# Kernel tuning notes

Hardware: AMD Instinct MI355X
Metric: run time of the kernel (lower is better)

## Reference

```python
import jax, jax.numpy as jnp
import numpy as np

B, L, D, H = 2, 1024, 512, 8
h = D // H            # head_dim = 64
K = H                 # num_eigh must equal num_heads (vmap pairing in conv)
EPS = 1e-5


def _spectral_filters(seq_len: int, k: int) -> np.ndarray:
    # Hankel matrix Z_{ij} = 2 / ((i+j)^3 - (i+j)), top-k eigenvectors scaled by sigma^{1/4}
    e = np.arange(1, seq_len + 1, dtype=np.float64)
    ipj = e[:, None] + e[None, :]
    Z = 2.0 / (ipj ** 3 - ipj)
    sigma, phi = np.linalg.eigh(Z)
    sigma_k = np.clip(sigma[-k:], 1e-9, None)
    return (phi[:, -k:] * sigma_k ** 0.25).astype(np.float32)  # [L, K]


def setup_inputs() -> dict:
    key = jax.random.key(0)
    ks = jax.random.split(key, 8)
    s = 0.02
    return {
        "x": jax.random.normal(ks[0], (B, L, D), jnp.float32),
        "spectral_basis": jnp.asarray(_spectral_filters(L, K)),       # [L, K]
        "wq_w": jax.random.normal(ks[1], (D, D), jnp.float32) * s,
        "wq_b": jnp.zeros((D,), jnp.float32),
        "wk_w": jax.random.normal(ks[2], (D, D), jnp.float32) * s,
        "wk_b": jnp.zeros((D,), jnp.float32),
        "wv_w": jax.random.normal(ks[3], (D, D), jnp.float32) * s,
        "wv_b": jnp.zeros((D,), jnp.float32),
        "wo_w": jax.random.normal(ks[4], (D, D), jnp.float32) * s,
        "wo_b": jnp.zeros((D,), jnp.float32),
        "wg_w": jax.random.normal(ks[5], (h * h,), jnp.float32) * s,  # Linear(h^2 -> 1)
        "wg_b": jnp.zeros((), jnp.float32),
    }


def _causal_fft_conv(u, filt_f, n):
    # u: [B,H,L,h]; filt_f: precomputed rfft of per-head filters [H, F]
    Uf = jnp.fft.rfft(u, n=n, axis=2)                        # [B,H,F,h]
    y = jnp.fft.irfft(Uf * filt_f[None, :, :, None], n=n, axis=2)
    return y[:, :, :L]                                       # truncate full conv -> causal


def reference(x, spectral_basis, wq_w, wq_b, wk_w, wk_b, wv_w, wv_b,
              wo_w, wo_b, wg_w, wg_b):
    # projections -> [B,H,L,h]
    q = (x @ wq_w + wq_b).reshape(B, L, H, h).transpose(0, 2, 1, 3)
    k = (x @ wk_w + wk_b).reshape(B, L, H, h).transpose(0, 2, 1, 3) * h ** (-0.5)
    v = (x @ wv_w + wv_b).reshape(B, L, H, h).transpose(0, 2, 1, 3)

    n = 2 * L
    filt_f = jnp.fft.rfft(spectral_basis.T, n=n, axis=1)     # [H, F] (one filter per head)
    k_conv = _causal_fft_conv(k, filt_f, n)
    v_conv = _causal_fft_conv(v, filt_f, n)

    # gated outer product Z: [B,H,L,h,h]
    Z = jnp.einsum('bhlm,bhln->bhlmn', v_conv, k_conv)
    gate_logits = Z.reshape(B, H, L, h * h) @ wg_w + wg_b    # [B,H,L]
    gates = jax.nn.relu(gate_logits) ** 2 + EPS
    gated_Z = gates[..., None, None] * Z

    # associative scan (additive) over sequence dim
    cumul_gated_Z = jnp.cumsum(gated_Z, axis=2)              # [B,H,L,h,h]
    cumul_gates = jnp.cumsum(gates, axis=2)                  # [B,H,L]
    attn = cumul_gated_Z / (cumul_gates[..., None, None] + EPS)

    # note: original einsum sums over l (and d) independently of s
    ctxt = jnp.einsum('bhsd,bhlde->bhse', q, attn)           # [B,H,L,h]
    norm = jnp.linalg.norm(ctxt, axis=3, keepdims=True)
    unit = ctxt / jnp.maximum(norm, EPS)                     # F.normalize semantics
    out = unit.transpose(0, 2, 1, 3).reshape(B, L, D)
    return out @ wo_w + wo_b
```

## Files before the change

kernel.cpp:

```cpp
#include <hip/hip_runtime.h>
#include <math.h>


typedef __attribute__((ext_vector_type(8))) short short8;
typedef __attribute__((ext_vector_type(4))) float floatx4;

__device__ __forceinline__ unsigned short f2bf(float f) {
    unsigned int u = __float_as_uint(f);
    unsigned int r = (u + 0x7FFFu + ((u >> 16) & 1u)) >> 16;
    return (unsigned short)r;
}

__global__ __launch_bounds__(256) void k_prep(
    const float* __restrict__ x,
    const float* __restrict__ wq, const float* __restrict__ wk,
    const float* __restrict__ wv, const float* __restrict__ wo,
    const float* __restrict__ wg,
    unsigned short* __restrict__ xb,
    unsigned short* __restrict__ wT, unsigned short* __restrict__ woT,
    unsigned short* __restrict__ wgb)
{
    __shared__ float sf[64][65];
    const int blk = blockIdx.x;
    const int tid = threadIdx.x;

    if (blk < 512) {
        const int gid = blk * 256 + tid;
        const float4* x4 = (const float4*)x;
        float4 a = x4[gid*2], b = x4[gid*2+1];
        uint4 o;
        o.x = f2bf(a.x) | ((unsigned)f2bf(a.y) << 16);
        o.y = f2bf(a.z) | ((unsigned)f2bf(a.w) << 16);
        o.z = f2bf(b.x) | ((unsigned)f2bf(b.y) << 16);
        o.w = f2bf(b.z) | ((unsigned)f2bf(b.w) << 16);
        ((uint4*)xb)[gid] = o;
    } else if (blk < 768) {
        const int t = blk - 512;
        const float* src; unsigned short* dst; int n0, c0, k0;
        if (t < 192) {
            int nt = t >> 3, kt = t & 7;
            n0 = nt * 64; k0 = kt * 64;
            int z = n0 >> 9; c0 = n0 & 511;
            src = (z == 0) ? wq : (z == 1) ? wk : wv;
            dst = wT;
        } else {
            int u = t - 192; int nt = u >> 3, kt = u & 7;
            n0 = nt * 64; c0 = n0; k0 = kt * 64;
            src = wo; dst = woT;
        }
        const int rr = tid >> 4, c4 = tid & 15;
        #pragma unroll
        for (int g = 0; g < 4; ++g) {
            int r = g*16 + rr;
            float4 v = *(const float4*)&src[(size_t)(k0 + r)*512 + c0 + c4*4];
            sf[r][c4*4+0]=v.x; sf[r][c4*4+1]=v.y; sf[r][c4*4+2]=v.z; sf[r][c4*4+3]=v.w;
        }
        __syncthreads();
        #pragma unroll
        for (int g = 0; g < 4; ++g) {
            int c = g*16 + rr;
            int kk = c4*4;
            ushort4 o;
            o.x = f2bf(sf[kk+0][c]); o.y = f2bf(sf[kk+1][c]);
            o.z = f2bf(sf[kk+2][c]); o.w = f2bf(sf[kk+3][c]);
            *(ushort4*)&dst[(size_t)(n0 + c)*512 + k0 + kk] = o;
        }
    } else {
        const float4* wg4 = (const float4*)wg;
        for (int i = tid; i < 512; i += 256) {
            float4 a = wg4[i*2], b = wg4[i*2+1];
            uint4 o;
            o.x = f2bf(a.x) | ((unsigned)f2bf(a.y) << 16);
            o.y = f2bf(a.z) | ((unsigned)f2bf(a.w) << 16);
            o.z = f2bf(b.x) | ((unsigned)f2bf(b.y) << 16);
            o.w = f2bf(b.z) | ((unsigned)f2bf(b.w) << 16);
            ((uint4*)wgb)[i] = o;
        }
    }
}

__global__ __launch_bounds__(256) void k_qkv_mfma(
    const unsigned short* __restrict__ xb, const unsigned short* __restrict__ wT,
    const float* __restrict__ bq, const float* __restrict__ bk,
    const float* __restrict__ bv,
    float* __restrict__ qo, unsigned short* __restrict__ ub2)
{
    const int tid = threadIdx.x;
    const int lane = tid & 63, wave = tid >> 6;
    const int q = lane >> 4, ln = lane & 15;
    const int wm = wave * 32;
    const int m0 = blockIdx.y * 128;
    const int n0 = blockIdx.x * 64;

    __shared__ unsigned short As[128*72];
    __shared__ unsigned short Bs[64*72];

    floatx4 acc[2][4];
    #pragma unroll
    for (int i = 0; i < 2; ++i)
        #pragma unroll
        for (int j = 0; j < 4; ++j)
            acc[i][j] = (floatx4){0.f, 0.f, 0.f, 0.f};

    const uint4* Ag = (const uint4*)xb;
    const uint4* Bg = (const uint4*)wT;
    for (int k0 = 0; k0 < 512; k0 += 64) {
        #pragma unroll
        for (int s = 0; s < 4; ++s) {
            int idx = s*256 + tid;
            int r = idx >> 3, cp = idx & 7;
            uint4 va = Ag[(size_t)(m0 + r)*64 + (k0 >> 3) + cp];
            *(uint4*)&As[r*72 + cp*8] = va;
        }
        #pragma unroll
        for (int s = 0; s < 2; ++s) {
            int idx = s*256 + tid;
            int r = idx >> 3, cp = idx & 7;
            uint4 vb = Bg[(size_t)(n0 + r)*64 + (k0 >> 3) + cp];
            *(uint4*)&Bs[r*72 + cp*8] = vb;
        }
        __syncthreads();
        short8 af0[2], af1[2], bf0[4], bf1[4];
        #pragma unroll
        for (int i = 0; i < 2; ++i) {
            af0[i] = *(const short8*)&As[(wm + i*16 + ln)*72 + q*8];
            af1[i] = *(const short8*)&As[(wm + i*16 + ln)*72 + 32 + q*8];
        }
        #pragma unroll
        for (int i = 0; i < 4; ++i) {
            bf0[i] = *(const short8*)&Bs[(i*16 + ln)*72 + q*8];
            bf1[i] = *(const short8*)&Bs[(i*16 + ln)*72 + 32 + q*8];
        }
        #pragma unroll
        for (int mi = 0; mi < 2; ++mi)
            #pragma unroll
            for (int ni = 0; ni < 4; ++ni) {
                acc[mi][ni] = __builtin_amdgcn_mfma_f32_16x16x32_bf16(
                    af0[mi], bf0[ni], acc[mi][ni], 0, 0, 0);
                acc[mi][ni] = __builtin_amdgcn_mfma_f32_16x16x32_bf16(
                    af1[mi], bf1[ni], acc[mi][ni], 0, 0, 0);
            }
        __syncthreads();
    }

    const int z = n0 >> 9;
    if (z == 0) {
        #pragma unroll
        for (int mi = 0; mi < 2; ++mi) {
            #pragma unroll
            for (int ni = 0; ni < 4; ++ni) {
                int c = (n0 + ni*16 + ln) & 511;
                int head = c >> 6, dd = c & 63;
                float bb = bq[c];
                #pragma unroll
                for (int reg = 0; reg < 4; ++reg) {
                    int row = m0 + wm + mi*16 + q*4 + reg;
                    int b = row >> 10, l = row & 1023;
                    qo[(size_t)((b*8 + head)*1024 + l)*64 + dd] =
                        acc[mi][ni][reg] + bb;
                }
            }
        }
    } else {
        const float scale = (z == 1) ? 0.125f : 1.0f;
        const float* bias = (z == 1) ? bk : bv;
        unsigned short* dst = ub2 + (size_t)(z-1) * 16 * 64 * 1024;
        #pragma unroll
        for (int mi = 0; mi < 2; ++mi) {
            #pragma unroll
            for (int ni = 0; ni < 4; ++ni) {
                int c = (n0 + ni*16 + ln) & 511;
                int head = c >> 6, dd = c & 63;
                float bb = bias[c];
                int row0 = m0 + wm + mi*16 + q*4;
                int b = row0 >> 10, l0 = row0 & 1023;
                ushort4 o;
                o.x = f2bf((acc[mi][ni][0] + bb) * scale);
                o.y = f2bf((acc[mi][ni][1] + bb) * scale);
                o.z = f2bf((acc[mi][ni][2] + bb) * scale);
                o.w = f2bf((acc[mi][ni][3] + bb) * scale);
                *(ushort4*)&dst[((size_t)((b*8 + head)*64) + dd)*1024 + l0] = o;
            }
        }
    }
}

__global__ __launch_bounds__(256) void k_conv_mfma(
    const float* __restrict__ sb,
    const unsigned short* __restrict__ ub2,
    float* __restrict__ kc, float* __restrict__ vc,
    unsigned short* __restrict__ kcb)
{
    const int tid = threadIdx.x;
    const int lane = tid & 63, wave = tid >> 6;
    const int q = lane >> 4, ln = lane & 15;
    const int bht = blockIdx.x;
    const int it  = blockIdx.y;
    const int t0  = it * 64;
    const int bh  = bht & 15, h = bh & 7, tensor = bht >> 4;

    __shared__ unsigned short revf[1152];
    __shared__ unsigned short Bs[64*72];

    for (int i = tid; i < 1152; i += 256) {
        int d = 1087 - i;
        revf[i] = (d >= 0 && d < 1024) ? f2bf(sb[d*8 + h]) : (unsigned short)0;
    }

    const uint4* Bg = (const uint4*)ub2;
    const size_t bbase = (size_t)bht * 8192;

    floatx4 acc[4];
    #pragma unroll
    for (int i = 0; i < 4; ++i) acc[i] = (floatx4){0.f,0.f,0.f,0.f};

    const int kend = t0 + 64;
    const int arow = 1087 - t0 - (wave*16 + ln);
    for (int k0 = 0; k0 < kend; k0 += 64) {
        #pragma unroll
        for (int s = 0; s < 2; ++s) {
            int idx = s*256 + tid;
            int r = idx >> 3, cp = idx & 7;
            uint4 vb = Bg[bbase + (size_t)r*128 + (k0 >> 3) + cp];
            *(uint4*)&Bs[r*72 + cp*8] = vb;
        }
        __syncthreads();
        const int ab = arow + k0 + q*8;
        short8 a0, a1;
        #pragma unroll
        for (int j = 0; j < 8; ++j) {
            a0[j] = (short)revf[ab + j];
            a1[j] = (short)revf[ab + 32 + j];
        }
        #pragma unroll
        for (int ni = 0; ni < 4; ++ni) {
            short8 b0 = *(const short8*)&Bs[(ni*16 + ln)*72 + q*8];
            short8 b1 = *(const short8*)&Bs[(ni*16 + ln)*72 + 32 + q*8];
            acc[ni] = __builtin_amdgcn_mfma_f32_16x16x32_bf16(a0, b0, acc[ni], 0, 0, 0);
            acc[ni] = __builtin_amdgcn_mfma_f32_16x16x32_bf16(a1, b1, acc[ni], 0, 0, 0);
        }
        __syncthreads();
    }

    float* dst = (tensor ? vc : kc) + (size_t)bh * 65536;
    #pragma unroll
    for (int ni = 0; ni < 4; ++ni)
        #pragma unroll
        for (int reg = 0; reg < 4; ++reg) {
            int row = t0 + wave*16 + q*4 + reg;
            dst[(size_t)row*64 + ni*16 + ln] = acc[ni][reg];
        }
    if (!tensor) {
        unsigned short* db = kcb + (size_t)bh * 65536;
        #pragma unroll
        for (int ni = 0; ni < 4; ++ni)
            #pragma unroll
            for (int reg = 0; reg < 4; ++reg) {
                int row = t0 + wave*16 + q*4 + reg;
                db[(size_t)row*64 + ni*16 + ln] = f2bf(acc[ni][reg]);
            }
    }
}

__global__ __launch_bounds__(256) void k_gate_mfma(
    const unsigned short* __restrict__ kcb, const float* __restrict__ vc,
    const unsigned short* __restrict__ wgb, const float* __restrict__ wg_b,
    float* __restrict__ gl)
{
    const int tid = threadIdx.x;
    const int lane = tid & 63, wave = tid >> 6;
    const int q = lane >> 4, ln = lane & 15;
    const int l0 = blockIdx.x * 64;
    const int bh = blockIdx.y;

    __shared__ unsigned short As[64*72];
    __shared__ unsigned short Bs[64*72];

    const uint4* Ag = (const uint4*)(kcb + (size_t)bh * 65536);
    const uint4* Bg = (const uint4*)wgb;
    #pragma unroll
    for (int s = 0; s < 2; ++s) {
        int idx = s*256 + tid;
        int r = idx >> 3, cp = idx & 7;
        *(uint4*)&As[r*72 + cp*8] = Ag[(size_t)(l0 + r)*8 + cp];
        *(uint4*)&Bs[r*72 + cp*8] = Bg[r*8 + cp];
    }
    __syncthreads();

    floatx4 T[4];
    #pragma unroll
    for (int mt = 0; mt < 4; ++mt) T[mt] = (floatx4){0.f,0.f,0.f,0.f};
    #pragma unroll
    for (int k0 = 0; k0 < 64; k0 += 32) {
        short8 a = *(const short8*)&As[(wave*16 + ln)*72 + k0 + q*8];
        #pragma unroll
        for (int mt = 0; mt < 4; ++mt) {
            short8 b = *(const short8*)&Bs[(mt*16 + ln)*72 + k0 + q*8];
            T[mt] = __builtin_amdgcn_mfma_f32_16x16x32_bf16(a, b, T[mt], 0, 0, 0);
        }
    }

    const float* vb = vc + (size_t)bh * 65536;
    float part[4] = {0.f, 0.f, 0.f, 0.f};
    #pragma unroll
    for (int mt = 0; mt < 4; ++mt)
        #pragma unroll
        for (int reg = 0; reg < 4; ++reg) {
            int l = l0 + wave*16 + q*4 + reg;
            part[reg] += T[mt][reg] * vb[(size_t)l*64 + mt*16 + ln];
        }
    #pragma unroll
    for (int reg = 0; reg < 4; ++reg) {
        part[reg] += __shfl_xor(part[reg], 1);
        part[reg] += __shfl_xor(part[reg], 2);
        part[reg] += __shfl_xor(part[reg], 4);
        part[reg] += __shfl_xor(part[reg], 8);
    }
    if (ln == 0) {
        const float wgbias = wg_b[0];
        #pragma unroll
        for (int reg = 0; reg < 4; ++reg) {
            int l = l0 + wave*16 + q*4 + reg;
            float s = part[reg] + wgbias;
            float rr = fmaxf(s, 0.0f);
            gl[bh*1024 + l] = rr*rr + 1e-5f;
        }
    }
}

__global__ __launch_bounds__(256) void k_amat(
    const float* __restrict__ kc, const float* __restrict__ vc,
    const float* __restrict__ gl, float* __restrict__ apart)
{
    const int tid = threadIdx.x, tx = tid & 15, ty = tid >> 4;
    const int bh = blockIdx.x, slc = blockIdx.y;
    const float* kb = kc + (size_t)bh * 65536;
    const float* vb = vc + (size_t)bh * 65536;

    __shared__ float sbuf[256];
    __shared__ float wfull[1024];
    __shared__ __align__(16) float vs[16][68];
    __shared__ __align__(16) float ks2[16][68];

    {
        const float4 g4 = ((const float4*)(gl + bh*1024))[tid];
        float g[4] = {g4.x, g4.y, g4.z, g4.w};
        float p[4];
        p[0]=g[0]; p[1]=p[0]+g[1]; p[2]=p[1]+g[2]; p[3]=p[2]+g[3];
        const float s = p[3];
        sbuf[tid] = s;
        __syncthreads();
        for (int off = 1; off < 256; off <<= 1) {
            float t = (tid >= off) ? sbuf[tid-off] : 0.0f;
            __syncthreads();
            sbuf[tid] += t;
            __syncthreads();
        }
        const float base = sbuf[tid] - s;
        float r[4], pr[4];
        #pragma unroll
        for (int u = 0; u < 4; ++u) r[u] = 1.0f / (base + p[u] + 1e-5f);
        pr[0]=r[0]; pr[1]=pr[0]+r[1]; pr[2]=pr[1]+r[2]; pr[3]=pr[2]+r[3];
        const float sr = pr[3];
        __syncthreads();
        sbuf[tid] = sr;
        __syncthreads();
        for (int off = 1; off < 256; off <<= 1) {
            float t = (tid >= off) ? sbuf[tid-off] : 0.0f;
            __syncthreads();
            sbuf[tid] += t;
            __syncthreads();
        }
        const float Rtot  = sbuf[255];
        const float baser = sbuf[tid] - sr;
        wfull[tid*4+0] = g[0] * (Rtot - (baser + pr[0]) + r[0]);
        wfull[tid*4+1] = g[1] * (Rtot - (baser + pr[1]) + r[1]);
        wfull[tid*4+2] = g[2] * (Rtot - (baser + pr[2]) + r[2]);
        wfull[tid*4+3] = g[3] * (Rtot - (baser + pr[3]) + r[3]);
    }
    __syncthreads();

    float acc[4][4] = {};
    const float4* k4 = (const float4*)kb;
    const float4* v4 = (const float4*)vb;
    for (int j0 = slc*128; j0 < slc*128 + 128; j0 += 16) {
        {
            int r = tid >> 4, c4 = tid & 15;
            *(float4*)&vs[r][c4*4]  = v4[(size_t)(j0 + r)*16 + c4];
            *(float4*)&ks2[r][c4*4] = k4[(size_t)(j0 + r)*16 + c4];
        }
        __syncthreads();
        #pragma unroll
        for (int jj = 0; jj < 16; ++jj) {
            float wj = wfull[j0 + jj];
            float a[4];
            a[0] = vs[jj][ty*4+0]*wj; a[1] = vs[jj][ty*4+1]*wj;
            a[2] = vs[jj][ty*4+2]*wj; a[3] = vs[jj][ty*4+3]*wj;
            float4 b4 = *(const float4*)&ks2[jj][tx*4];
            float bb[4] = {b4.x, b4.y, b4.z, b4.w};
            #pragma unroll
            for (int ii = 0; ii < 4; ++ii)
                #pragma unroll
                for (int jc = 0; jc < 4; ++jc)
                    acc[ii][jc] += a[ii] * bb[jc];
        }
        __syncthreads();
    }
    float* ap = apart + (size_t)(slc*16 + bh) * 4096;
    #pragma unroll
    for (int i = 0; i < 4; ++i) {
        float4 o = { acc[i][0], acc[i][1], acc[i][2], acc[i][3] };
        *(float4*)&ap[(ty*4+i)*64 + tx*4] = o;
    }
}

__global__ __launch_bounds__(256) void k_ctxt(
    const float* __restrict__ q, const float* __restrict__ apart,
    unsigned short* __restrict__ ub)
{
    const int tid = threadIdx.x, tx = tid & 15, ty = tid >> 4;
    const int l0 = blockIdx.x * 64;
    const int bh = blockIdx.y;
    const float* qb = q + (size_t)bh * 65536;

    __shared__ __align__(16) float qs[64][20];
    __shared__ __align__(16) float As[16][68];
    float acc[4][4] = {};
    const float4* q4 = (const float4*)qb;
    const float4* a4 = (const float4*)apart;
    for (int d0 = 0; d0 < 64; d0 += 16) {
        {
            int r = tid >> 2, c4 = tid & 3;
            float4 t = q4[(size_t)(l0 + r)*16 + (d0 >> 2) + c4];
            *(float4*)&qs[r][c4*4] = t;
        }
        {
            int r = tid >> 4, c4 = tid & 15;
            size_t o = (size_t)(d0 + r)*16 + c4;
            float4 t = a4[(size_t)(0*16 + bh)*1024 + o];
            #pragma unroll
            for (int s = 1; s < 8; ++s) {
                float4 u = a4[(size_t)(s*16 + bh)*1024 + o];
                t.x += u.x; t.y += u.y; t.z += u.z; t.w += u.w;
            }
            *(float4*)&As[r][c4*4] = t;
        }
        __syncthreads();
        float qreg[4][16];
        #pragma unroll
        for (int i = 0; i < 4; ++i)
            #pragma unroll
            for (int c = 0; c < 4; ++c) {
                float4 t = *(const float4*)&qs[ty*4+i][c*4];
                qreg[i][c*4+0] = t.x; qreg[i][c*4+1] = t.y;
                qreg[i][c*4+2] = t.z; qreg[i][c*4+3] = t.w;
            }
        #pragma unroll
        for (int dd = 0; dd < 16; ++dd) {
            float4 b4 = *(const float4*)&As[dd][tx*4];
            float bb[4] = {b4.x, b4.y, b4.z, b4.w};
            #pragma unroll
            for (int ii = 0; ii < 4; ++ii)
                #pragma unroll
                for (int jj = 0; jj < 4; ++jj)
                    acc[ii][jj] += qreg[ii][dd] * bb[jj];
        }
        __syncthreads();
    }
    __shared__ float red[64][17];
    __shared__ float nrm[64];
    #pragma unroll
    for (int i = 0; i < 4; ++i) {
        red[ty*4+i][tx] = acc[i][0]*acc[i][0] + acc[i][1]*acc[i][1]
                        + acc[i][2]*acc[i][2] + acc[i][3]*acc[i][3];
    }
    __syncthreads();
    if (tid < 64) {
        float s = 0.0f;
        #pragma unroll
        for (int t = 0; t < 16; ++t) s += red[tid][t];
        nrm[tid] = fmaxf(sqrtf(s), 1e-5f);
    }
    __syncthreads();
    const int b = bh >> 3, hd = bh & 7;
    #pragma unroll
    for (int i = 0; i < 4; ++i) {
        int lr = ty*4 + i;
        float inv = 1.0f / nrm[lr];
        ushort4 o;
        o.x = f2bf(acc[i][0]*inv); o.y = f2bf(acc[i][1]*inv);
        o.z = f2bf(acc[i][2]*inv); o.w = f2bf(acc[i][3]*inv);
        *(ushort4*)&ub[(size_t)(b*1024 + l0 + lr)*512 + hd*64 + tx*4] = o;
    }
}

__global__ __launch_bounds__(256) void k_out_mfma(
    const unsigned short* __restrict__ ub, const unsigned short* __restrict__ woT,
    const float* __restrict__ bo, float* __restrict__ out)
{
    const int tid = threadIdx.x;
    const int lane = tid & 63, wave = tid >> 6;
    const int q = lane >> 4, ln = lane & 15;
    const int wm = wave * 32;
    const int m0 = blockIdx.y * 128;
    const int n0 = blockIdx.x * 64;

    __shared__ unsigned short As[128*72];
    __shared__ unsigned short Bs[64*72];

    floatx4 acc[2][4];
    #pragma unroll
    for (int i = 0; i < 2; ++i)
        #pragma unroll
        for (int j = 0; j < 4; ++j)
            acc[i][j] = (floatx4){0.f, 0.f, 0.f, 0.f};

    const uint4* Ag = (const uint4*)ub;
    const uint4* Bg = (const uint4*)woT;
    for (int k0 = 0; k0 < 512; k0 += 64) {
        #pragma unroll
        for (int s = 0; s < 4; ++s) {
            int idx = s*256 + tid;
            int r = idx >> 3, cp = idx & 7;
            uint4 va = Ag[(size_t)(m0 + r)*64 + (k0 >> 3) + cp];
            *(uint4*)&As[r*72 + cp*8] = va;
        }
        #pragma unroll
        for (int s = 0; s < 2; ++s) {
            int idx = s*256 + tid;
            int r = idx >> 3, cp = idx & 7;
            uint4 vb = Bg[(size_t)(n0 + r)*64 + (k0 >> 3) + cp];
            *(uint4*)&Bs[r*72 + cp*8] = vb;
        }
        __syncthreads();
        short8 af0[2], af1[2], bf0[4], bf1[4];
        #pragma unroll
        for (int i = 0; i < 2; ++i) {
            af0[i] = *(const short8*)&As[(wm + i*16 + ln)*72 + q*8];
            af1[i] = *(const short8*)&As[(wm + i*16 + ln)*72 + 32 + q*8];
        }
        #pragma unroll
        for (int i = 0; i < 4; ++i) {
            bf0[i] = *(const short8*)&Bs[(i*16 + ln)*72 + q*8];
            bf1[i] = *(const short8*)&Bs[(i*16 + ln)*72 + 32 + q*8];
        }
        #pragma unroll
        for (int mi = 0; mi < 2; ++mi)
            #pragma unroll
            for (int ni = 0; ni < 4; ++ni) {
                acc[mi][ni] = __builtin_amdgcn_mfma_f32_16x16x32_bf16(
                    af0[mi], bf0[ni], acc[mi][ni], 0, 0, 0);
                acc[mi][ni] = __builtin_amdgcn_mfma_f32_16x16x32_bf16(
                    af1[mi], bf1[ni], acc[mi][ni], 0, 0, 0);
            }
        __syncthreads();
    }

    #pragma unroll
    for (int mi = 0; mi < 2; ++mi) {
        #pragma unroll
        for (int ni = 0; ni < 4; ++ni) {
            int gcol = n0 + ni*16 + ln;
            float bb = bo[gcol];
            #pragma unroll
            for (int reg = 0; reg < 4; ++reg) {
                int row = m0 + wm + mi*16 + q*4 + reg;
                out[(size_t)row*512 + gcol] = acc[mi][ni][reg] + bb;
            }
        }
    }
}

extern "C" void kernel_launch(void* const* d_in, const int* in_sizes, int n_in,
                              void* d_out, int out_size, void* d_ws, size_t ws_size,
                              hipStream_t stream)
{
    const float* x   = (const float*)d_in[0];
    const float* sb  = (const float*)d_in[1];
    const float* wq  = (const float*)d_in[2];
    const float* bq  = (const float*)d_in[3];
    const float* wk  = (const float*)d_in[4];
    const float* bk  = (const float*)d_in[5];
    const float* wv  = (const float*)d_in[6];
    const float* bv  = (const float*)d_in[7];
    const float* wo  = (const float*)d_in[8];
    const float* bo  = (const float*)d_in[9];
    const float* wg  = (const float*)d_in[10];
    const float* wgb = (const float*)d_in[11];
    float* out = (float*)d_out;
    float* ws  = (float*)d_ws;

    float* Q   = ws;
    float* KC  = ws + 1048576;
    float* VC  = ws + 2*1048576;
    float* GL  = ws + 3*1048576;
    float* AP  = GL + 16384;
    float* fp  = AP + 524288;
    unsigned short* XB  = (unsigned short*)fp;
    unsigned short* WT  = XB  + 1048576;
    unsigned short* WOT = WT  + 786432;
    unsigned short* UB  = WOT + 262144;
    unsigned short* UB2 = UB  + 1048576;
    unsigned short* WGB = UB2 + 2097152;
    unsigned short* KCB = WGB + 4096;

    k_prep     <<<dim3(769),    256, 0, stream>>>(x, wq, wk, wv, wo, wg,
                                                  XB, WT, WOT, WGB);
    k_qkv_mfma <<<dim3(24, 16), 256, 0, stream>>>(XB, WT, bq, bk, bv, Q, UB2);
    k_conv_mfma<<<dim3(32, 16), 256, 0, stream>>>(sb, UB2, KC, VC, KCB);
    k_gate_mfma<<<dim3(16, 16), 256, 0, stream>>>(KCB, VC, WGB, wgb, GL);
    k_amat     <<<dim3(16, 8),  256, 0, stream>>>(KC, VC, GL, AP);
    k_ctxt     <<<dim3(16, 16), 256, 0, stream>>>(Q, AP, UB);
    k_out_mfma <<<dim3(8, 16),  256, 0, stream>>>(UB, WOT, bo, out);
}
```

Measured before the change: 149.2 us.

## Fuse conv and gate kernels, use wave-shuffle scans, split amat finer

Merges the k and v causal convolutions and the gate computation into one kernel. Each block now computes both k_conv and v_conv tiles, sharing the filter A-fragments, and computes gate logits from registers and LDS, so the bf16 k copy and the v reload from global memory are no longer needed. The block-wide Hillis-Steele scans in k_amat are replaced with wave shuffle scans plus a small cross-wave combine, which removes many barriers. The amat reduction is split into 16 slices instead of 8 for more parallelism, at the cost of k_ctxt summing twice as many partials. The fused conv grid halves the block count and doubles the per-block MFMA and LDS work, which may reduce occupancy.

```diff
diff --git a/kernel.cpp b/kernel.cpp
--- a/kernel.cpp
+++ b/kernel.cpp
@@ -185,105 +185,92 @@
     }
 }
 
-__global__ __launch_bounds__(256) void k_conv_mfma(
+__global__ __launch_bounds__(256) void k_conv_gate(
     const float* __restrict__ sb,
     const unsigned short* __restrict__ ub2,
+    const unsigned short* __restrict__ wgb, const float* __restrict__ wg_b,
     float* __restrict__ kc, float* __restrict__ vc,
-    unsigned short* __restrict__ kcb)
-{
-    const int tid = threadIdx.x;
-    const int lane = tid & 63, wave = tid >> 6;
-    const int q = lane >> 4, ln = lane & 15;
-    const int bht = blockIdx.x;
-    const int it  = blockIdx.y;
-    const int t0  = it * 64;
-    const int bh  = bht & 15, h = bh & 7, tensor = bht >> 4;
-
-    __shared__ unsigned short revf[1152];
-    __shared__ unsigned short Bs[64*72];
-
-    for (int i = tid; i < 1152; i += 256) {
-        int d = 1087 - i;
-        revf[i] = (d >= 0 && d < 1024) ? f2bf(sb[d*8 + h]) : (unsigned short)0;
-    }
-
-    const uint4* Bg = (const uint4*)ub2;
-    const size_t bbase = (size_t)bht * 8192;
-
-    floatx4 acc[4];
-    #pragma unroll
-    for (int i = 0; i < 4; ++i) acc[i] = (floatx4){0.f,0.f,0.f,0.f};
-
-    const int kend = t0 + 64;
-    const int arow = 1087 - t0 - (wave*16 + ln);
-    for (int k0 = 0; k0 < kend; k0 += 64) {
-        #pragma unroll
-        for (int s = 0; s < 2; ++s) {
-            int idx = s*256 + tid;
-            int r = idx >> 3, cp = idx & 7;
-            uint4 vb = Bg[bbase + (size_t)r*128 + (k0 >> 3) + cp];
-            *(uint4*)&Bs[r*72 + cp*8] = vb;
-        }
-        __syncthreads();
-        const int ab = arow + k0 + q*8;
-        short8 a0, a1;
-        #pragma unroll
-        for (int j = 0; j < 8; ++j) {
-            a0[j] = (short)revf[ab + j];
-            a1[j] = (short)revf[ab + 32 + j];
-        }
-        #pragma unroll
-        for (int ni = 0; ni < 4; ++ni) {
-            short8 b0 = *(const short8*)&Bs[(ni*16 + ln)*72 + q*8];
-            short8 b1 = *(const short8*)&Bs[(ni*16 + ln)*72 + 32 + q*8];
-            acc[ni] = __builtin_amdgcn_mfma_f32_16x16x32_bf16(a0, b0, acc[ni], 0, 0, 0);
-            acc[ni] = __builtin_amdgcn_mfma_f32_16x16x32_bf16(a1, b1, acc[ni], 0, 0, 0);
-        }
-        __syncthreads();
-    }
-
-    float* dst = (tensor ? vc : kc) + (size_t)bh * 65536;
-    #pragma unroll
-    for (int ni = 0; ni < 4; ++ni)
-        #pragma unroll
-        for (int reg = 0; reg < 4; ++reg) {
-            int row = t0 + wave*16 + q*4 + reg;
-            dst[(size_t)row*64 + ni*16 + ln] = acc[ni][reg];
-        }
-    if (!tensor) {
-        unsigned short* db = kcb + (size_t)bh * 65536;
-        #pragma unroll
-        for (int ni = 0; ni < 4; ++ni)
-            #pragma unroll
-            for (int reg = 0; reg < 4; ++reg) {
-                int row = t0 + wave*16 + q*4 + reg;
-                db[(size_t)row*64 + ni*16 + ln] = f2bf(acc[ni][reg]);
-            }
-    }
-}
-
-__global__ __launch_bounds__(256) void k_gate_mfma(
-    const unsigned short* __restrict__ kcb, const float* __restrict__ vc,
-    const unsigned short* __restrict__ wgb, const float* __restrict__ wg_b,
     float* __restrict__ gl)
 {
     const int tid = threadIdx.x;
     const int lane = tid & 63, wave = tid >> 6;
     const int q = lane >> 4, ln = lane & 15;
-    const int l0 = blockIdx.x * 64;
-    const int bh = blockIdx.y;
-
-    __shared__ unsigned short As[64*72];
-    __shared__ unsigned short Bs[64*72];
-
-    const uint4* Ag = (const uint4*)(kcb + (size_t)bh * 65536);
-    const uint4* Bg = (const uint4*)wgb;
-    #pragma unroll
-    for (int s = 0; s < 2; ++s) {
-        int idx = s*256 + tid;
-        int r = idx >> 3, cp = idx & 7;
-        *(uint4*)&As[r*72 + cp*8] = Ag[(size_t)(l0 + r)*8 + cp];
-        *(uint4*)&Bs[r*72 + cp*8] = Bg[r*8 + cp];
+    const int bh  = blockIdx.x, h = bh & 7;
+    const int it  = blockIdx.y;
+    const int t0  = it * 64;
+
+    __shared__ unsigned short revf[1152];
+    __shared__ unsigned short Bk[64*72];
+    __shared__ unsigned short Bv[64*72];
+
+    for (int i = tid; i < 1152; i += 256) {
+        int d = 1087 - i;
+        revf[i] = (d >= 0 && d < 1024) ? f2bf(sb[d*8 + h]) : (unsigned short)0;
+    }
+
+    const uint4* Bg = (const uint4*)ub2;
+    const size_t bk_base = (size_t)bh * 8192;
+    const size_t bv_base = (size_t)(16 + bh) * 8192;
+
+    floatx4 acck[4], accv[4];
+    #pragma unroll
+    for (int i = 0; i < 4; ++i) {
+        acck[i] = (floatx4){0.f,0.f,0.f,0.f};
+        accv[i] = (floatx4){0.f,0.f,0.f,0.f};
+    }
+
+    const int kend = t0 + 64;
+    const int arow = 1087 - t0 - (wave*16 + ln);
+    for (int k0 = 0; k0 < kend; k0 += 64) {
+        #pragma unroll
+        for (int s = 0; s < 2; ++s) {
+            int idx = s*256 + tid;
+            int r = idx >> 3, cp = idx & 7;
+            *(uint4*)&Bk[r*72 + cp*8] = Bg[bk_base + (size_t)r*128 + (k0 >> 3) + cp];
+            *(uint4*)&Bv[r*72 + cp*8] = Bg[bv_base + (size_t)r*128 + (k0 >> 3) + cp];
+        }
+        __syncthreads();
+        const int ab = arow + k0 + q*8;
+        short8 a0, a1;
+        #pragma unroll
+        for (int j = 0; j < 8; ++j) {
+            a0[j] = (short)revf[ab + j];
+            a1[j] = (short)revf[ab + 32 + j];
+        }
+        #pragma unroll
+        for (int ni = 0; ni < 4; ++ni) {
+            short8 kb0 = *(const short8*)&Bk[(ni*16 + ln)*72 + q*8];
+            short8 kb1 = *(const short8*)&Bk[(ni*16 + ln)*72 + 32 + q*8];
+            short8 vb0 = *(const short8*)&Bv[(ni*16 + ln)*72 + q*8];
+            short8 vb1 = *(const short8*)&Bv[(ni*16 + ln)*72 + 32 + q*8];
+            acck[ni] = __builtin_amdgcn_mfma_f32_16x16x32_bf16(a0, kb0, acck[ni], 0, 0, 0);
+            acck[ni] = __builtin_amdgcn_mfma_f32_16x16x32_bf16(a1, kb1, acck[ni], 0, 0, 0);
+            accv[ni] = __builtin_amdgcn_mfma_f32_16x16x32_bf16(a0, vb0, accv[ni], 0, 0, 0);
+            accv[ni] = __builtin_amdgcn_mfma_f32_16x16x32_bf16(a1, vb1, accv[ni], 0, 0, 0);
+        }
+        __syncthreads();
+    }
+
+    float* kdst = kc + (size_t)bh * 65536;
+    float* vdst = vc + (size_t)bh * 65536;
+    #pragma unroll
+    for (int ni = 0; ni < 4; ++ni)
+        #pragma unroll
+        for (int reg = 0; reg < 4; ++reg) {
+            int row = wave*16 + q*4 + reg;
+            int grow = t0 + row;
+            kdst[(size_t)grow*64 + ni*16 + ln] = acck[ni][reg];
+            vdst[(size_t)grow*64 + ni*16 + ln] = accv[ni][reg];
+            Bk[row*72 + ni*16 + ln] = f2bf(acck[ni][reg]);
+        }
+    {
+        const uint4* Wg = (const uint4*)wgb;
+        #pragma unroll
+        for (int s = 0; s < 2; ++s) {
+            int idx = s*256 + tid;
+            int r = idx >> 3, cp = idx & 7;
+            *(uint4*)&Bv[r*72 + cp*8] = Wg[r*8 + cp];
+        }
     }
     __syncthreads();
 
@@ -291,24 +278,21 @@
     #pragma unroll
     for (int mt = 0; mt < 4; ++mt) T[mt] = (floatx4){0.f,0.f,0.f,0.f};
     #pragma unroll
-    for (int k0 = 0; k0 < 64; k0 += 32) {
-        short8 a = *(const short8*)&As[(wave*16 + ln)*72 + k0 + q*8];
+    for (int k0g = 0; k0g < 64; k0g += 32) {
+        short8 a = *(const short8*)&Bk[(wave*16 + ln)*72 + k0g + q*8];
         #pragma unroll
         for (int mt = 0; mt < 4; ++mt) {
-            short8 b = *(const short8*)&Bs[(mt*16 + ln)*72 + k0 + q*8];
+            short8 b = *(const short8*)&Bv[(mt*16 + ln)*72 + k0g + q*8];
             T[mt] = __builtin_amdgcn_mfma_f32_16x16x32_bf16(a, b, T[mt], 0, 0, 0);
         }
     }
 
-    const float* vb = vc + (size_t)bh * 65536;
     float part[4] = {0.f, 0.f, 0.f, 0.f};
     #pragma unroll
     for (int mt = 0; mt < 4; ++mt)
         #pragma unroll
-        for (int reg = 0; reg < 4; ++reg) {
-            int l = l0 + wave*16 + q*4 + reg;
-            part[reg] += T[mt][reg] * vb[(size_t)l*64 + mt*16 + ln];
-        }
+        for (int reg = 0; reg < 4; ++reg)
+            part[reg] += T[mt][reg] * accv[mt][reg];
     #pragma unroll
     for (int reg = 0; reg < 4; ++reg) {
         part[reg] += __shfl_xor(part[reg], 1);
@@ -320,7 +304,7 @@
         const float wgbias = wg_b[0];
         #pragma unroll
         for (int reg = 0; reg < 4; ++reg) {
-            int l = l0 + wave*16 + q*4 + reg;
+            int l = t0 + wave*16 + q*4 + reg;
             float s = part[reg] + wgbias;
             float rr = fmaxf(s, 0.0f);
             gl[bh*1024 + l] = rr*rr + 1e-5f;
@@ -333,11 +317,12 @@
     const float* __restrict__ gl, float* __restrict__ apart)
 {
     const int tid = threadIdx.x, tx = tid & 15, ty = tid >> 4;
+    const int lane = tid & 63, wave = tid >> 6;
     const int bh = blockIdx.x, slc = blockIdx.y;
     const float* kb = kc + (size_t)bh * 65536;
     const float* vb = vc + (size_t)bh * 65536;
 
-    __shared__ float sbuf[256];
+    __shared__ float scanA[4], scanB[4];
     __shared__ float wfull[1024];
     __shared__ __align__(16) float vs[16][68];
     __shared__ __align__(16) float ks2[16][68];
@@ -347,32 +332,38 @@
         float g[4] = {g4.x, g4.y, g4.z, g4.w};
         float p[4];
         p[0]=g[0]; p[1]=p[0]+g[1]; p[2]=p[1]+g[2]; p[3]=p[2]+g[3];
-        const float s = p[3];
-        sbuf[tid] = s;
-        __syncthreads();
-        for (int off = 1; off < 256; off <<= 1) {
-            float t = (tid >= off) ? sbuf[tid-off] : 0.0f;
-            __syncthreads();
-            sbuf[tid] += t;
-            __syncthreads();
-        }
-        const float base = sbuf[tid] - s;
+        float x = p[3];
+        #pragma unroll
+        for (int off = 1; off < 64; off <<= 1) {
+            float t = __shfl_up(x, off);
+            if (lane >= off) x += t;
+        }
+        if (lane == 63) scanA[wave] = x;
+        __syncthreads();
+        float wb = 0.f;
+        #pragma unroll
+        for (int wv = 0; wv < 4; ++wv) wb += (wv < wave) ? scanA[wv] : 0.f;
+        const float base = wb + x - p[3];
         float r[4], pr[4];
         #pragma unroll
         for (int u = 0; u < 4; ++u) r[u] = 1.0f / (base + p[u] + 1e-5f);
         pr[0]=r[0]; pr[1]=pr[0]+r[1]; pr[2]=pr[1]+r[2]; pr[3]=pr[2]+r[3];
-        const float sr = pr[3];
-        __syncthreads();
-        sbuf[tid] = sr;
-        __syncthreads();
-        for (int off = 1; off < 256; off <<= 1) {
-            float t = (tid >= off) ? sbuf[tid-off] : 0.0f;
-            __syncthreads();
-            sbuf[tid] += t;
-            __syncthreads();
-        }
-        const float Rtot  = sbuf[255];
-        const float baser = sbuf[tid] - sr;
+        float y = pr[3];
+        #pragma unroll
+        for (int off = 1; off < 64; off <<= 1) {
+            float t = __shfl_up(y, off);
+            if (lane >= off) y += t;
+        }
+        if (lane == 63) scanB[wave] = y;
+        __syncthreads();
+        float rb = 0.f, Rtot = 0.f;
+        #pragma unroll
+        for (int wv = 0; wv < 4; ++wv) {
+            rb   += (wv < wave) ? scanB[wv] : 0.f;
+            Rtot += scanB[wv];
+        }
+        const float baser = rb + y - pr[3];
+        wfull[tid*4+0] = g[0] * (Rtot - (baser + pr[0] - pr[3]) - pr[3] + pr[3] - (pr[0] - r[0]) - r[0] + r[0]);
         wfull[tid*4+0] = g[0] * (Rtot - (baser + pr[0]) + r[0]);
         wfull[tid*4+1] = g[1] * (Rtot - (baser + pr[1]) + r[1]);
         wfull[tid*4+2] = g[2] * (Rtot - (baser + pr[2]) + r[2]);
@@ -383,7 +374,7 @@
     float acc[4][4] = {};
     const float4* k4 = (const float4*)kb;
     const float4* v4 = (const float4*)vb;
-    for (int j0 = slc*128; j0 < slc*128 + 128; j0 += 16) {
+    for (int j0 = slc*64; j0 < slc*64 + 64; j0 += 16) {
         {
             int r = tid >> 4, c4 = tid & 15;
             *(float4*)&vs[r][c4*4]  = v4[(size_t)(j0 + r)*16 + c4];
@@ -439,7 +430,7 @@
             size_t o = (size_t)(d0 + r)*16 + c4;
             float4 t = a4[(size_t)(0*16 + bh)*1024 + o];
             #pragma unroll
-            for (int s = 1; s < 8; ++s) {
+            for (int s = 1; s < 16; ++s) {
                 float4 u = a4[(size_t)(s*16 + bh)*1024 + o];
                 t.x += u.x; t.y += u.y; t.z += u.z; t.w += u.w;
             }
@@ -595,21 +586,19 @@
     float* VC  = ws + 2*1048576;
     float* GL  = ws + 3*1048576;
     float* AP  = GL + 16384;
-    float* fp  = AP + 524288;
+    float* fp  = AP + 1048576;
     unsigned short* XB  = (unsigned short*)fp;
     unsigned short* WT  = XB  + 1048576;
     unsigned short* WOT = WT  + 786432;
     unsigned short* UB  = WOT + 262144;
     unsigned short* UB2 = UB  + 1048576;
     unsigned short* WGB = UB2 + 2097152;
-    unsigned short* KCB = WGB + 4096;
 
     k_prep     <<<dim3(769),    256, 0, stream>>>(x, wq, wk, wv, wo, wg,
                                                   XB, WT, WOT, WGB);
     k_qkv_mfma <<<dim3(24, 16), 256, 0, stream>>>(XB, WT, bq, bk, bv, Q, UB2);
-    k_conv_mfma<<<dim3(32, 16), 256, 0, stream>>>(sb, UB2, KC, VC, KCB);
-    k_gate_mfma<<<dim3(16, 16), 256, 0, stream>>>(KCB, VC, WGB, wgb, GL);
-    k_amat     <<<dim3(16, 8),  256, 0, stream>>>(KC, VC, GL, AP);
+    k_conv_gate<<<dim3(16, 16), 256, 0, stream>>>(sb, UB2, WGB, wgb, KC, VC, GL);
+    k_amat     <<<dim3(16, 16), 256, 0, stream>>>(KC, VC, GL, AP);
     k_ctxt     <<<dim3(16, 16), 256, 0, stream>>>(Q, AP, UB);
     k_out_mfma <<<dim3(8, 16),  256, 0, stream>>>(UB, WOT, bo, out);
 }
```

Result: faster. 143.7 us (-3.7%).
